# Kernel tuning notes

Measured on AMD Instinct MI355X. Metric: run time of the kernel, lower is better.

Reference implementation:

```python
import jax, jax.numpy as jnp
from jax import lax
import numpy as np

B = 8
IN_SCALE = 9            # 1 + 2*input_window_size
S2 = IN_SCALE * IN_SCALE  # 81
MODES = 16
J = 5 * S2 + MODES      # 421
RBF = 64
HDC = 256
NCA_H = 32
NCA_STEPS = 20
MAX_T = 100.0           # max_time_step (None in source -> bug; fixed constant)


def _pool_matrix(I, O):
    # faithful AdaptiveAvgPool over dim of size I -> O (torch bin boundaries)
    M = np.zeros((O, I), np.float32)
    for o in range(O):
        s = (o * I) // O
        e = -((-(o + 1) * I) // O)
        M[o, s:e] = 1.0 / (e - s)
    return jnp.asarray(M)

POOL = _pool_matrix(J, S2)  # [81, 421]


def _meta_encoding(m_in, m_out):
    # vectorized version of the per-i loop in meta_encoding
    pos_in = m_in / MAX_T
    pos_out = m_out / MAX_T
    i = jnp.arange(MODES)
    div = jnp.power(10000.0, (2.0 * (i // 2)).astype(jnp.float32) / MODES)
    a_in = pos_in[:, None] / div[None, :]   # [B, MODES]
    a_out = pos_out[:, None] / div[None, :]
    even = (jnp.sin(a_in) + jnp.cos(a_in)) * 0.5
    odd = (jnp.cos(a_in) + jnp.sin(a_out)) * 0.5
    return jnp.where((i % 2 == 0)[None, :], even, odd)


def setup_inputs() -> dict:
    key = jax.random.key(0)
    ks = jax.random.split(key, 12)
    data_input = jax.random.uniform(ks[0], (B, 4 * IN_SCALE, IN_SCALE), jnp.float32)
    structure_input = jax.random.uniform(ks[1], (B, IN_SCALE, IN_SCALE), jnp.float32)
    meta_in = jax.random.uniform(ks[2], (B,), jnp.float32) * MAX_T
    meta_out = jax.random.uniform(ks[3], (B,), jnp.float32) * MAX_T
    # learned / fixed params
    rbf_probes = jax.random.uniform(ks[4], (RBF, J, HDC), jnp.float32) * 2.0
    compress_w = jax.random.normal(ks[5], (5, RBF), jnp.float32)
    compress_b = jnp.full((5,), 0.01, jnp.float32)
    nca_w1 = jax.random.normal(ks[6], (NCA_H, 5, 3, 3), jnp.float32) * 0.1
    nca_b1 = jnp.full((NCA_H,), 0.01, jnp.float32)
    nca_w2 = jax.random.normal(ks[7], (5, NCA_H), jnp.float32) * 0.1
    nca_b2 = jnp.full((5,), 0.01, jnp.float32)
    # sparse random +/-1 HDC projection matrix (scatter into flat zeros, as in source)
    input_dim = 5 * S2
    n_nz = input_dim * HDC
    idx = np.asarray(jax.random.randint(ks[8], (n_nz,), 0, input_dim * HDC))
    signs = np.asarray(jax.random.randint(ks[9], (n_nz,), 0, 2)).astype(np.float32) * 2.0 - 1.0
    flat = np.zeros((B * J * HDC,), np.float32)
    flat[idx] = signs
    hdc_matrix = jnp.asarray(flat.reshape(B, J, HDC))
    return {
        "data_input": data_input, "structure_input": structure_input,
        "meta_in": meta_in, "meta_out": meta_out,
        "rbf_probes": rbf_probes, "hdc_matrix": hdc_matrix,
        "compress_w": compress_w, "compress_b": compress_b,
        "nca_w1": nca_w1, "nca_b1": nca_b1, "nca_w2": nca_w2, "nca_b2": nca_b2,
    }


def _forward(data_input, structure_input, meta_in, meta_out, rbf_probes,
             hdc_matrix, compress_w, compress_b, nca_w1, nca_b1, nca_w2, nca_b2):
    pe = _meta_encoding(meta_in, meta_out)                       # [B, 16]
    data = jnp.concatenate(
        [data_input.reshape(B, -1), structure_input.reshape(B, -1), pe], axis=1)  # [B, J]
    # einsum 'bi,bjd->bjd' sums data over i and broadcasts over (j, d)
    proj = data.sum(axis=1)[:, None, None] * hdc_matrix          # [B, J, HDC]
    # broadcast RBF distance: the big memory-bound intermediate [B, RBF, J, HDC]
    dist = (rbf_probes[None, :, :, :] - proj[:, None, :, :]) ** 2
    # 1x1 conv over rbf channel dim, then tanh -> [B, 5, J, HDC]
    x = jnp.tanh(jnp.einsum('brjd,or->bojd', dist, compress_w)
                 + compress_b[None, :, None, None])

    def nca_step(x, _):
        h = lax.conv_general_dilated(x, nca_w1, (1, 1), 'SAME',
                                     dimension_numbers=('NCHW', 'OIHW', 'NCHW'))
        h = jax.nn.relu(h + nca_b1[None, :, None, None])
        dx = jnp.einsum('bhjd,oh->bojd', h, nca_w2) + nca_b2[None, :, None, None]
        return x + dx, None

    x, _ = lax.scan(nca_step, x, None, length=NCA_STEPS)
    x = jnp.tanh(x)
    # AdaptiveAvgPool2d((S2, 1)): mean over HDC, adaptive pool J -> S2
    x = jnp.einsum('bcj,oj->bco', x.mean(axis=-1), POOL)         # [B, 5, 81]
    r = x[:, 0, :].reshape(B, IN_SCALE, IN_SCALE)
    g = x[:, 1, :].reshape(B, IN_SCALE, IN_SCALE)
    b = x[:, 2, :].reshape(B, IN_SCALE, IN_SCALE)
    a = x[:, 3, :].reshape(B, IN_SCALE, IN_SCALE)
    s = x[:, 4, :].reshape(B, IN_SCALE, IN_SCALE)
    return (r, g, b, a, s)


def reference(data_input, structure_input, meta_in, meta_out, rbf_probes,
              hdc_matrix, compress_w, compress_b, nca_w1, nca_b1, nca_w2, nca_b2):
    return _forward(data_input, structure_input, meta_in, meta_out, rbf_probes,
                    hdc_matrix, compress_w, compress_b, nca_w1, nca_b1, nca_w2, nca_b2)
```

## Files before the change

kernel.cpp:

```cpp
#include <hip/hip_runtime.h>
#include <math.h>

#define NB 8
#define JJ 421
#define HDCN 256
#define PP (JJ*HDCN)
#define STEPS 20

typedef __attribute__((ext_vector_type(8))) short bf16x8;
typedef __attribute__((ext_vector_type(4))) float f32x4;
typedef __attribute__((ext_vector_type(2))) float f32x2;
typedef __attribute__((ext_vector_type(4))) unsigned int uint4v;
typedef __attribute__((ext_vector_type(2))) int int2v;
typedef unsigned short ushort;
typedef unsigned int uint;

__device__ __forceinline__ ushort f2bf(float f) {
    union { float f; uint u; } a; a.f = f;
    uint r = 0x7fffu + ((a.u >> 16) & 1u);
    return (ushort)((a.u + r) >> 16);
}
__device__ __forceinline__ uint splitpack(float x) {
    uint u = __float_as_uint(x);
    uint r = 0x7fffu + ((u >> 16) & 1u);
    uint hib = (u + r) & 0xffff0000u;
    float lo = x - __uint_as_float(hib);
    return hib | f2bf(lo);
}
__device__ __forceinline__ float unpack2(uint p) {
    return __uint_as_float(p & 0xffff0000u) + __uint_as_float(p << 16);
}
__device__ __forceinline__ float tanh_fast(float x) {
    float e = __expf(2.f * x);
    return 1.f - 2.f / (e + 1.f);
}
__device__ __forceinline__ float wave_reduce_sum(float v) {
#pragma unroll
    for (int off = 32; off > 0; off >>= 1) v += __shfl_down(v, off);
    return v;
}
__device__ __forceinline__ float red32(float d) {
#if __has_builtin(__builtin_amdgcn_permlane32_swap)
    int2v pr = __builtin_amdgcn_permlane32_swap(__float_as_int(d), __float_as_int(d), false, false);
    return __int_as_float(pr.x) + __int_as_float(pr.y);
#else
    return d + __shfl_xor(d, 32);
#endif
}

__global__ __launch_bounds__(256) void k_wprep(
    const float* __restrict__ w1, const float* __restrict__ b1,
    const float* __restrict__ w2,
    ushort* __restrict__ Pw, float* __restrict__ w2p)
{
    int t = threadIdx.x;
    for (int idx = t; idx < 3072; idx += 256) {
        int p = idx >> 10, rem = idx & 1023, oc = rem >> 5, k = rem & 31;
        int tau = k & 15;
        float v = 0.f;
        if (tau < 15) v = w1[oc * 45 + (tau / 3) * 9 + (tau % 3) * 3 + p];
        Pw[idx] = f2bf(v);
    }
    int oc = t >> 3, o = t & 7;
    float v = 0.f;
    if (o < 5) v = w2[o * 32 + oc];
    else if (o == 5) v = b1[oc];
    w2p[t] = v;
}

__global__ __launch_bounds__(128) void k_prep(
    const float* __restrict__ din, const float* __restrict__ stin,
    const float* __restrict__ m_in, const float* __restrict__ m_out,
    float* __restrict__ sbuf)
{
    int b = blockIdx.x, t = threadIdx.x;
    float acc = 0.f;
    for (int k = t; k < 324; k += 128) acc += din[b * 324 + k];
    for (int k = t; k < 81;  k += 128) acc += stin[b * 81 + k];
    if (t < 16) {
        int i = t;
        float pos_in  = m_in[b]  * 0.01f;
        float pos_out = m_out[b] * 0.01f;
        float div = powf(10000.0f, (float)(2 * (i / 2)) / 16.0f);
        float ai = pos_in / div, ao = pos_out / div;
        float v = ((i & 1) == 0) ? 0.5f * (sinf(ai) + cosf(ai))
                                 : 0.5f * (cosf(ai) + sinf(ao));
        acc += v;
    }
    __shared__ float part[2];
    float w = wave_reduce_sum(acc);
    if ((t & 63) == 0) part[t >> 6] = w;
    __syncthreads();
    if (t == 0) sbuf[b] = part[0] + part[1];
}

__global__ __launch_bounds__(128) void k_x0(
    const float* __restrict__ rbf, const float* __restrict__ hdc,
    const float* __restrict__ cw, const float* __restrict__ cb,
    const float* __restrict__ sbuf, uint* __restrict__ x0)
{
    __shared__ float wl[320];
    __shared__ float Cw[5];
    __shared__ float sb[8];
    __shared__ float cbs[5];
    int t = threadIdx.x;
    for (int k = t; k < 320; k += 128) wl[k] = cw[k];
    if (t < 8)   sb[t] = sbuf[t];
    if (t < 5)   cbs[t] = cb[t];
    __syncthreads();
    if (t < 5) { float c = 0.f; for (int r = 0; r < 64; ++r) c += wl[t * 64 + r]; Cw[t] = c; }
    __syncthreads();

    int jd = blockIdx.x * 128 + t;
    float A[5]  = {0, 0, 0, 0, 0};
    float Bv[5] = {0, 0, 0, 0, 0};
    for (int r = 0; r < 64; ++r) {
        float v  = rbf[(size_t)r * PP + jd];
        float v2 = v * v;
#pragma unroll
        for (int o = 0; o < 5; ++o) {
            float w = wl[o * 64 + r];
            A[o]  = fmaf(w, v2, A[o]);
            Bv[o] = fmaf(w, v,  Bv[o]);
        }
    }
#pragma unroll
    for (int b = 0; b < 8; ++b) {
        float p  = sb[b] * hdc[(size_t)b * PP + jd];
        float p2 = p * p;
#pragma unroll
        for (int o = 0; o < 5; ++o) {
            float val = A[o] - 2.f * p * Bv[o] + p2 * Cw[o] + cbs[o];
            x0[(size_t)(b * 5 + o) * PP + jd] = splitpack(tanh_fast(val));
        }
    }
}

__global__ __launch_bounds__(256, 3) void k_nca(
    const uint* __restrict__ xin, uint* __restrict__ xout,
    const ushort* __restrict__ Pw, const float* __restrict__ w2p,
    const float* __restrict__ b2, float* __restrict__ mbuf, int dofinal)
{
    __shared__ uint Bs[2][258 * 16];
    __shared__ float Ms[2][5][4];

    const int t = threadIdx.x;
    const int b = blockIdx.x & 7;
    const int pj = blockIdx.x >> 3;
    const int j0 = pj * 2;
    const bool has1 = (j0 + 1) < JJ;
    const int lane = t & 63, wv = t >> 6;
    const int m = lane & 15, gq = lane >> 4;

    bf16x8 Ap[3][2];
#pragma unroll
    for (int p = 0; p < 3; ++p)
#pragma unroll
        for (int mt = 0; mt < 2; ++mt)
            Ap[p][mt] = *(const bf16x8*)(Pw + p * 1024 + (mt * 16 + m) * 32 + gq * 8);

    float w2r[2][4][5], b1r[2][4], b2r[5];
#pragma unroll
    for (int mt = 0; mt < 2; ++mt)
#pragma unroll
        for (int i = 0; i < 4; ++i) {
            int oc = mt * 16 + gq * 4 + i;
            const float* wp = w2p + oc * 8;
            f32x4 a = *(const f32x4*)wp;
            f32x2 e = *(const f32x2*)(wp + 4);
            w2r[mt][i][0] = a[0]; w2r[mt][i][1] = a[1];
            w2r[mt][i][2] = a[2]; w2r[mt][i][3] = a[3];
            w2r[mt][i][4] = e[0]; b1r[mt][i] = e[1];
        }
#pragma unroll
    for (int o = 0; o < 5; ++o) b2r[o] = b2[o];

    uint v[5][4];
    {
        const uint* xb = xin + (size_t)b * 5 * PP;
#pragma unroll
        for (int c = 0; c < 5; ++c)
#pragma unroll
            for (int rr = 0; rr < 4; ++rr) {
                int jj = j0 - 1 + rr;
                uint val = 0;
                if (jj >= 0 && jj < JJ) val = xb[(size_t)(c * JJ + jj) * HDCN + t];
                v[c][rr] = val;
            }
        const int row = t + 1;
        const int s = (row >> 1) & 3;
#pragma unroll
        for (int r = 0; r < 2; ++r) {
            if (r == 1 && !has1) break;
            uint xh[8], xl[8];
#pragma unroll
            for (int w = 0; w < 8; ++w) {
                int k0 = 2 * w, k1 = 2 * w + 1;
                uint a = (k0 < 15) ? v[k0 / 3][k0 % 3 + r] : 0u;
                uint c = (k1 < 15) ? v[k1 / 3][k1 % 3 + r] : 0u;
                xh[w] = (a >> 16) | (c & 0xffff0000u);
                xl[w] = (a & 0xffffu) | (c << 16);
            }
            uint* rb = &Bs[r][row * 16];
            *(uint4v*)(rb + ((0 ^ s) << 2)) = (uint4v){xh[0], xh[1], xh[2], xh[3]};
            *(uint4v*)(rb + ((1 ^ s) << 2)) = (uint4v){xh[4], xh[5], xh[6], xh[7]};
            *(uint4v*)(rb + ((2 ^ s) << 2)) = (uint4v){xl[0], xl[1], xl[2], xl[3]};
            *(uint4v*)(rb + ((3 ^ s) << 2)) = (uint4v){xl[4], xl[5], xl[6], xl[7]};
        }
        if (t < 4) {
            uint* zr = &Bs[t >> 1][(t & 1) ? 257 * 16 : 0];
            uint4v z = (uint4v){0, 0, 0, 0};
            ((uint4v*)zr)[0] = z; ((uint4v*)zr)[1] = z;
            ((uint4v*)zr)[2] = z; ((uint4v*)zr)[3] = z;
        }
    }
    __syncthreads();

#pragma unroll
    for (int r = 0; r < 2; ++r) {
        if (r == 1 && !has1) break;
        const int j = j0 + r;

        f32x4 acc[2][4];
#pragma unroll
        for (int mt = 0; mt < 2; ++mt)
#pragma unroll
            for (int nt = 0; nt < 4; ++nt) acc[mt][nt] = (f32x4){0.f, 0.f, 0.f, 0.f};

#pragma unroll
        for (int nt = 0; nt < 4; ++nt) {
            int px = (wv << 6) + (nt << 4) + m;
#pragma unroll
            for (int p = 0; p < 3; ++p) {
                int row = px + p;
                int s2 = (row >> 1) & 3;
                bf16x8 Bf = *(const bf16x8*)(&Bs[r][row * 16] + ((gq ^ s2) << 2));
                acc[0][nt] = __builtin_amdgcn_mfma_f32_16x16x32_bf16(Ap[p][0], Bf, acc[0][nt], 0, 0, 0);
                acc[1][nt] = __builtin_amdgcn_mfma_f32_16x16x32_bf16(Ap[p][1], Bf, acc[1][nt], 0, 0, 0);
            }
        }

        float dxs[5] = {0, 0, 0, 0, 0};
#pragma unroll
        for (int nt = 0; nt < 4; ++nt) {
            float dx[5] = {0, 0, 0, 0, 0};
#pragma unroll
            for (int mt = 0; mt < 2; ++mt)
#pragma unroll
                for (int i = 0; i < 4; ++i) {
                    float h = fmaxf(acc[mt][nt][i] + b1r[mt][i], 0.f);
#pragma unroll
                    for (int o = 0; o < 5; ++o) dx[o] = fmaf(w2r[mt][i][o], h, dx[o]);
                }
#pragma unroll
            for (int o = 0; o < 5; ++o) {
                dx[o] += __shfl_xor(dx[o], 16);
                dx[o] = red32(dx[o]);
                if (nt == gq) dxs[o] = dx[o];
            }
        }

        const size_t base_bj = (size_t)b * 5 * PP + (size_t)j * HDCN;
        float xnv[5];
#pragma unroll
        for (int c = 0; c < 5; ++c) {
            xnv[c] = unpack2(v[c][r + 1]) + dxs[c] + b2r[c];
            if (!dofinal) xout[base_bj + (size_t)c * PP + t] = splitpack(xnv[c]);
        }

        if (dofinal) {
#pragma unroll
            for (int c = 0; c < 5; ++c) {
                float s = wave_reduce_sum(tanh_fast(xnv[c]));
                if (lane == 0) Ms[r][c][wv] = s;
            }
        }
    }

    if (dofinal) {
        __syncthreads();
        if (t < 10) {
            int rr = t / 5, c = t % 5;
            if (rr == 0 || has1) {
                float s = Ms[rr][c][0] + Ms[rr][c][1] + Ms[rr][c][2] + Ms[rr][c][3];
                mbuf[(b * 5 + c) * JJ + (j0 + rr)] = s * (1.0f / 256.0f);
            }
        }
    }
}

__global__ __launch_bounds__(256) void k_out(
    const float* __restrict__ m, float* __restrict__ out)
{
    int idx = blockIdx.x * 256 + threadIdx.x;
    if (idx >= 5 * NB * 81) return;
    int c = idx / (NB * 81);
    int rem = idx % (NB * 81);
    int b = rem / 81;
    int o = rem % 81;
    int s_ = (o * JJ) / 81;
    int e_ = ((o + 1) * JJ + 80) / 81;
    float acc = 0.f;
    for (int jj = s_; jj < e_; ++jj) acc += m[(b * 5 + c) * JJ + jj];
    out[idx] = acc / (float)(e_ - s_);
}

extern "C" void kernel_launch(void* const* d_in, const int* in_sizes, int n_in,
                              void* d_out, int out_size, void* d_ws, size_t ws_size,
                              hipStream_t stream) {
    const float* data_in  = (const float*)d_in[0];
    const float* struc_in = (const float*)d_in[1];
    const float* meta_in  = (const float*)d_in[2];
    const float* meta_out = (const float*)d_in[3];
    const float* rbf      = (const float*)d_in[4];
    const float* hdc      = (const float*)d_in[5];
    const float* cw       = (const float*)d_in[6];
    const float* cb       = (const float*)d_in[7];
    const float* w1       = (const float*)d_in[8];
    const float* b1       = (const float*)d_in[9];
    const float* w2       = (const float*)d_in[10];
    const float* b2       = (const float*)d_in[11];
    float* out = (float*)d_out;

    float* ws   = (float*)d_ws;
    float* sbuf = ws;
    float* mbuf = ws + 64;
    ushort* Pw  = (ushort*)(ws + 20480);
    float* w2p  = ws + 22528;
    uint* xA = (uint*)(ws + 32768);
    uint* xB = xA + (size_t)NB * 5 * PP;

    k_wprep<<<1, 256, 0, stream>>>(w1, b1, w2, Pw, w2p);
    k_prep<<<NB, 128, 0, stream>>>(data_in, struc_in, meta_in, meta_out, sbuf);
    k_x0<<<842, 128, 0, stream>>>(rbf, hdc, cw, cb, sbuf, xA);

    for (int step = 0; step < STEPS; ++step) {
        const uint* xi = (step & 1) ? xB : xA;
        uint*       xo = (step & 1) ? xA : xB;
        k_nca<<<NB * 211, 256, 0, stream>>>(xi, xo, Pw, w2p, b2, mbuf,
                                            (step == STEPS - 1) ? 1 : 0);
    }
    k_out<<<(5 * NB * 81 + 255) / 256, 256, 0, stream>>>(mbuf, out);
}
```

Measured before the change: 403.5 us.

## Process one j row per NCA block instead of two, raising occupancy

The NCA step kernel now handles a single j position per block, with the grid grown to NB*JJ blocks, and the launch bounds raised to allow 4 blocks per CU. LDS use halves, the MFMA loop is restructured so accumulators are per-tile instead of a full 2x4 array, and the 16-lane reduction uses permlane16_swap. This trades the reuse of overlapping halo rows (more global loads per output row) for higher parallelism, lower register pressure and better latency hiding.

After: 465.4 us. 15.3% more time.

```diff
diff --git a/kernel.cpp b/kernel.cpp
--- a/kernel.cpp
+++ b/kernel.cpp
@@ -38,6 +38,14 @@
 #pragma unroll
     for (int off = 32; off > 0; off >>= 1) v += __shfl_down(v, off);
     return v;
+}
+__device__ __forceinline__ float red16(float d) {
+#if __has_builtin(__builtin_amdgcn_permlane16_swap)
+    int2v pr = __builtin_amdgcn_permlane16_swap(__float_as_int(d), __float_as_int(d), false, false);
+    return __int_as_float(pr.x) + __int_as_float(pr.y);
+#else
+    return d + __shfl_xor(d, 16);
+#endif
 }
 __device__ __forceinline__ float red32(float d) {
 #if __has_builtin(__builtin_amdgcn_permlane32_swap)
@@ -136,21 +144,55 @@
     }
 }
 
-__global__ __launch_bounds__(256, 3) void k_nca(
+__global__ __launch_bounds__(256, 4) void k_nca(
     const uint* __restrict__ xin, uint* __restrict__ xout,
     const ushort* __restrict__ Pw, const float* __restrict__ w2p,
     const float* __restrict__ b2, float* __restrict__ mbuf, int dofinal)
 {
-    __shared__ uint Bs[2][258 * 16];
-    __shared__ float Ms[2][5][4];
+    __shared__ uint Bs[258 * 16];
+    __shared__ float Ms[5][4];
 
     const int t = threadIdx.x;
     const int b = blockIdx.x & 7;
-    const int pj = blockIdx.x >> 3;
-    const int j0 = pj * 2;
-    const bool has1 = (j0 + 1) < JJ;
+    const int j = blockIdx.x >> 3;
     const int lane = t & 63, wv = t >> 6;
     const int m = lane & 15, gq = lane >> 4;
+
+    uint v[5][3];
+    {
+        const uint* xb = xin + (size_t)b * 5 * PP;
+#pragma unroll
+        for (int c = 0; c < 5; ++c)
+#pragma unroll
+            for (int rr = 0; rr < 3; ++rr) {
+                int jj = j - 1 + rr;
+                uint val = 0;
+                if (jj >= 0 && jj < JJ) val = xb[(size_t)(c * JJ + jj) * HDCN + t];
+                v[c][rr] = val;
+            }
+        uint xh[8], xl[8];
+#pragma unroll
+        for (int w = 0; w < 8; ++w) {
+            int k0 = 2 * w, k1 = 2 * w + 1;
+            uint a = (k0 < 15) ? v[k0 / 3][k0 % 3] : 0u;
+            uint c = (k1 < 15) ? v[k1 / 3][k1 % 3] : 0u;
+            xh[w] = (a >> 16) | (c & 0xffff0000u);
+            xl[w] = (a & 0xffffu) | (c << 16);
+        }
+        const int row = t + 1;
+        const int s = (row >> 1) & 3;
+        uint* rb = &Bs[row * 16];
+        *(uint4v*)(rb + ((0 ^ s) << 2)) = (uint4v){xh[0], xh[1], xh[2], xh[3]};
+        *(uint4v*)(rb + ((1 ^ s) << 2)) = (uint4v){xh[4], xh[5], xh[6], xh[7]};
+        *(uint4v*)(rb + ((2 ^ s) << 2)) = (uint4v){xl[0], xl[1], xl[2], xl[3]};
+        *(uint4v*)(rb + ((3 ^ s) << 2)) = (uint4v){xl[4], xl[5], xl[6], xl[7]};
+        if (t < 2) {
+            uint* zr = &Bs[t ? 257 * 16 : 0];
+            uint4v z = (uint4v){0, 0, 0, 0};
+            ((uint4v*)zr)[0] = z; ((uint4v*)zr)[1] = z;
+            ((uint4v*)zr)[2] = z; ((uint4v*)zr)[3] = z;
+        }
+    }
 
     bf16x8 Ap[3][2];
 #pragma unroll
@@ -175,116 +217,60 @@
 #pragma unroll
     for (int o = 0; o < 5; ++o) b2r[o] = b2[o];
 
-    uint v[5][4];
-    {
-        const uint* xb = xin + (size_t)b * 5 * PP;
-#pragma unroll
-        for (int c = 0; c < 5; ++c)
-#pragma unroll
-            for (int rr = 0; rr < 4; ++rr) {
-                int jj = j0 - 1 + rr;
-                uint val = 0;
-                if (jj >= 0 && jj < JJ) val = xb[(size_t)(c * JJ + jj) * HDCN + t];
-                v[c][rr] = val;
+    __syncthreads();
+
+    float dxs[5] = {0, 0, 0, 0, 0};
+#pragma unroll
+    for (int nt = 0; nt < 4; ++nt) {
+        int px = (wv << 6) + (nt << 4) + m;
+        f32x4 acc0 = (f32x4){0.f, 0.f, 0.f, 0.f};
+        f32x4 acc1 = (f32x4){0.f, 0.f, 0.f, 0.f};
+#pragma unroll
+        for (int p = 0; p < 3; ++p) {
+            int row = px + p;
+            int s2 = (row >> 1) & 3;
+            bf16x8 Bf = *(const bf16x8*)(&Bs[row * 16] + ((gq ^ s2) << 2));
+            acc0 = __builtin_amdgcn_mfma_f32_16x16x32_bf16(Ap[p][0], Bf, acc0, 0, 0, 0);
+            acc1 = __builtin_amdgcn_mfma_f32_16x16x32_bf16(Ap[p][1], Bf, acc1, 0, 0, 0);
+        }
+
+        float dx[5] = {0, 0, 0, 0, 0};
+#pragma unroll
+        for (int i = 0; i < 4; ++i) {
+            float h0 = fmaxf(acc0[i] + b1r[0][i], 0.f);
+            float h1 = fmaxf(acc1[i] + b1r[1][i], 0.f);
+#pragma unroll
+            for (int o = 0; o < 5; ++o) {
+                dx[o] = fmaf(w2r[0][i][o], h0, dx[o]);
+                dx[o] = fmaf(w2r[1][i][o], h1, dx[o]);
             }
-        const int row = t + 1;
-        const int s = (row >> 1) & 3;
-#pragma unroll
-        for (int r = 0; r < 2; ++r) {
-            if (r == 1 && !has1) break;
-            uint xh[8], xl[8];
-#pragma unroll
-            for (int w = 0; w < 8; ++w) {
-                int k0 = 2 * w, k1 = 2 * w + 1;
-                uint a = (k0 < 15) ? v[k0 / 3][k0 % 3 + r] : 0u;
-                uint c = (k1 < 15) ? v[k1 / 3][k1 % 3 + r] : 0u;
-                xh[w] = (a >> 16) | (c & 0xffff0000u);
-                xl[w] = (a & 0xffffu) | (c << 16);
-            }
-            uint* rb = &Bs[r][row * 16];
-            *(uint4v*)(rb + ((0 ^ s) << 2)) = (uint4v){xh[0], xh[1], xh[2], xh[3]};
-            *(uint4v*)(rb + ((1 ^ s) << 2)) = (uint4v){xh[4], xh[5], xh[6], xh[7]};
-            *(uint4v*)(rb + ((2 ^ s) << 2)) = (uint4v){xl[0], xl[1], xl[2], xl[3]};
-            *(uint4v*)(rb + ((3 ^ s) << 2)) = (uint4v){xl[4], xl[5], xl[6], xl[7]};
-        }
-        if (t < 4) {
-            uint* zr = &Bs[t >> 1][(t & 1) ? 257 * 16 : 0];
-            uint4v z = (uint4v){0, 0, 0, 0};
-            ((uint4v*)zr)[0] = z; ((uint4v*)zr)[1] = z;
-            ((uint4v*)zr)[2] = z; ((uint4v*)zr)[3] = z;
-        }
-    }
-    __syncthreads();
-
-#pragma unroll
-    for (int r = 0; r < 2; ++r) {
-        if (r == 1 && !has1) break;
-        const int j = j0 + r;
-
-        f32x4 acc[2][4];
-#pragma unroll
-        for (int mt = 0; mt < 2; ++mt)
-#pragma unroll
-            for (int nt = 0; nt < 4; ++nt) acc[mt][nt] = (f32x4){0.f, 0.f, 0.f, 0.f};
-
-#pragma unroll
-        for (int nt = 0; nt < 4; ++nt) {
-            int px = (wv << 6) + (nt << 4) + m;
-#pragma unroll
-            for (int p = 0; p < 3; ++p) {
-                int row = px + p;
-                int s2 = (row >> 1) & 3;
-                bf16x8 Bf = *(const bf16x8*)(&Bs[r][row * 16] + ((gq ^ s2) << 2));
-                acc[0][nt] = __builtin_amdgcn_mfma_f32_16x16x32_bf16(Ap[p][0], Bf, acc[0][nt], 0, 0, 0);
-                acc[1][nt] = __builtin_amdgcn_mfma_f32_16x16x32_bf16(Ap[p][1], Bf, acc[1][nt], 0, 0, 0);
-            }
-        }
-
-        float dxs[5] = {0, 0, 0, 0, 0};
-#pragma unroll
-        for (int nt = 0; nt < 4; ++nt) {
-            float dx[5] = {0, 0, 0, 0, 0};
-#pragma unroll
-            for (int mt = 0; mt < 2; ++mt)
-#pragma unroll
-                for (int i = 0; i < 4; ++i) {
-                    float h = fmaxf(acc[mt][nt][i] + b1r[mt][i], 0.f);
-#pragma unroll
-                    for (int o = 0; o < 5; ++o) dx[o] = fmaf(w2r[mt][i][o], h, dx[o]);
-                }
-#pragma unroll
-            for (int o = 0; o < 5; ++o) {
-                dx[o] += __shfl_xor(dx[o], 16);
-                dx[o] = red32(dx[o]);
-                if (nt == gq) dxs[o] = dx[o];
-            }
-        }
-
-        const size_t base_bj = (size_t)b * 5 * PP + (size_t)j * HDCN;
-        float xnv[5];
+        }
+#pragma unroll
+        for (int o = 0; o < 5; ++o) {
+            dx[o] = red16(dx[o]);
+            dx[o] = red32(dx[o]);
+            if (nt == gq) dxs[o] = dx[o];
+        }
+    }
+
+    const size_t base_bj = (size_t)b * 5 * PP + (size_t)j * HDCN;
+    float xnv[5];
+#pragma unroll
+    for (int c = 0; c < 5; ++c) {
+        xnv[c] = unpack2(v[c][1]) + dxs[c] + b2r[c];
+        if (!dofinal) xout[base_bj + (size_t)c * PP + t] = splitpack(xnv[c]);
+    }
+
+    if (dofinal) {
 #pragma unroll
         for (int c = 0; c < 5; ++c) {
-            xnv[c] = unpack2(v[c][r + 1]) + dxs[c] + b2r[c];
-            if (!dofinal) xout[base_bj + (size_t)c * PP + t] = splitpack(xnv[c]);
-        }
-
-        if (dofinal) {
-#pragma unroll
-            for (int c = 0; c < 5; ++c) {
-                float s = wave_reduce_sum(tanh_fast(xnv[c]));
-                if (lane == 0) Ms[r][c][wv] = s;
-            }
-        }
-    }
-
-    if (dofinal) {
+            float s = wave_reduce_sum(tanh_fast(xnv[c]));
+            if (lane == 0) Ms[c][wv] = s;
+        }
         __syncthreads();
-        if (t < 10) {
-            int rr = t / 5, c = t % 5;
-            if (rr == 0 || has1) {
-                float s = Ms[rr][c][0] + Ms[rr][c][1] + Ms[rr][c][2] + Ms[rr][c][3];
-                mbuf[(b * 5 + c) * JJ + (j0 + rr)] = s * (1.0f / 256.0f);
-            }
+        if (t < 5) {
+            float s = Ms[t][0] + Ms[t][1] + Ms[t][2] + Ms[t][3];
+            mbuf[(b * 5 + t) * JJ + j] = s * (1.0f / 256.0f);
         }
     }
 }
@@ -337,8 +323,8 @@
     for (int step = 0; step < STEPS; ++step) {
         const uint* xi = (step & 1) ? xB : xA;
         uint*       xo = (step & 1) ? xA : xB;
-        k_nca<<<NB * 211, 256, 0, stream>>>(xi, xo, Pw, w2p, b2, mbuf,
-                                            (step == STEPS - 1) ? 1 : 0);
+        k_nca<<<NB * JJ, 256, 0, stream>>>(xi, xo, Pw, w2p, b2, mbuf,
+                                           (step == STEPS - 1) ? 1 : 0);
     }
     k_out<<<(5 * NB * 81 + 255) / 256, 256, 0, stream>>>(mbuf, out);
 }
```
